# Performance work log

Measured on AMD Instinct MI355X. Metric: run time of the kernel, lower is better.

The kernel has to match this reference:

```python
import jax, jax.numpy as jnp
from jax import lax
import numpy as np

B, T, D_IN, H, OUT = 64, 512, 512, 1024, 128


def setup_inputs() -> dict:
    key = jax.random.key(0)
    ks = jax.random.split(key, 12)
    s = 0.02
    return {
        "x": jax.random.normal(ks[0], (B, T, D_IN), dtype=jnp.float32),
        "W_ih0": jax.random.normal(ks[1], (H, D_IN), dtype=jnp.float32) * s,
        "W_hh0": jax.random.normal(ks[2], (H, H), dtype=jnp.float32) * s,
        "b_ih0": jax.random.normal(ks[3], (H,), dtype=jnp.float32) * s,
        "b_hh0": jax.random.normal(ks[4], (H,), dtype=jnp.float32) * s,
        "W_ih1": jax.random.normal(ks[5], (H, H), dtype=jnp.float32) * s,
        "W_hh1": jax.random.normal(ks[6], (H, H), dtype=jnp.float32) * s,
        "b_ih1": jax.random.normal(ks[7], (H,), dtype=jnp.float32) * s,
        "b_hh1": jax.random.normal(ks[8], (H,), dtype=jnp.float32) * s,
        "W_fc": jax.random.normal(ks[9], (OUT, H), dtype=jnp.float32) * s,
        "b_fc": jax.random.normal(ks[10], (OUT,), dtype=jnp.float32) * s,
    }


def _rnn_layer(seq, W_ih, W_hh, b_ih, b_hh):
    # seq: [B, T, D] -> outputs [B, T, H]; h_t = tanh(x_t W_ih^T + b_ih + h_{t-1} W_hh^T + b_hh)
    pre = jnp.einsum("btd,hd->bth", seq, W_ih) + b_ih + b_hh  # one big input GEMM
    h0 = jnp.zeros((seq.shape[0], W_hh.shape[0]), dtype=seq.dtype)

    def step(h, p_t):
        h_new = jnp.tanh(p_t + h @ W_hh.T)
        return h_new, h_new

    _, hs = lax.scan(step, h0, jnp.swapaxes(pre, 0, 1))  # [T, B, H]
    return jnp.swapaxes(hs, 0, 1)  # [B, T, H]


def reference(x, W_ih0, W_hh0, b_ih0, b_hh0, W_ih1, W_hh1, b_ih1, b_hh1, W_fc, b_fc):
    h1 = _rnn_layer(x, W_ih0, W_hh0, b_ih0, b_hh0)
    h2 = _rnn_layer(h1, W_ih1, W_hh1, b_ih1, b_hh1)
    last = h2[:, -1, :]  # [B, H]
    return last @ W_fc.T + b_fc  # [B, OUT]
```

## Files before the change

kernel.cpp:

```cpp
#include <hip/hip_runtime.h>
#include <stdint.h>
#include <stddef.h>

#define Bn   64
#define Tn   512
#define DINn 512
#define Hn   1024
#define OUTn 128

typedef __attribute__((ext_vector_type(4))) float f32x4;
typedef __attribute__((ext_vector_type(8))) short short8;
typedef __attribute__((ext_vector_type(4))) unsigned int u32x4;

__device__ __forceinline__ unsigned short f2bf(float f){
  unsigned int x = __builtin_bit_cast(unsigned int, f);
  x += 0x7fffu + ((x >> 16) & 1u);
  return (unsigned short)(x >> 16);
}
__device__ __forceinline__ float bf2f(unsigned short u){
  return __builtin_bit_cast(float, (unsigned int)u << 16);
}
__device__ __forceinline__ float tanh_fast(float v){
  float e = __expf(2.0f * v);
  return 1.0f - 2.0f / (e + 1.0f);
}

template<bool FAST>
__device__ __forceinline__ void st16(unsigned short* p, u32x4 v){
  if constexpr (FAST)
    asm volatile("global_store_dwordx4 %0, %1, off sc0" :: "v"(p), "v"(v) : "memory");
  else
    asm volatile("global_store_dwordx4 %0, %1, off sc0 sc1" :: "v"(p), "v"(v) : "memory");
}
__device__ __forceinline__ unsigned atom_poll(unsigned int* p){
  unsigned old, zero = 0;
  asm volatile("global_atomic_add %0, %1, %2, off sc0\n\t"
               "s_waitcnt vmcnt(0)"
               : "=&v"(old) : "v"(p), "v"(zero) : "memory");
  return old;
}
__device__ __forceinline__ void atom_poll2(unsigned int* p1, unsigned int* p2,
                                           unsigned &v1, unsigned &v2){
  unsigned zero = 0;
  asm volatile("global_atomic_add %0, %2, %4, off sc0\n\t"
               "global_atomic_add %1, %3, %4, off sc0\n\t"
               "s_waitcnt vmcnt(0)"
               : "=&v"(v1), "=&v"(v2)
               : "v"(p1), "v"(p2), "v"(zero) : "memory");
}
__device__ __forceinline__ void atom_inc(unsigned int* p){
  unsigned one = 1;
  asm volatile("global_atomic_add %0, %1, off" :: "v"(p), "v"(one) : "memory");
}
__device__ __forceinline__ unsigned ld1_sc0(const unsigned int* p){
  unsigned v;
  asm volatile("global_load_dword %0, %1, off sc0\n\t"
               "s_waitcnt vmcnt(0)" : "=&v"(v) : "v"(p) : "memory");
  return v;
}
__device__ __forceinline__ unsigned ld1_nt(const unsigned int* p){
  unsigned v;
  asm volatile("global_load_dword %0, %1, off nt\n\t"
               "s_waitcnt vmcnt(0)" : "=&v"(v) : "v"(p) : "memory");
  return v;
}
__device__ __forceinline__ unsigned umin4(u32x4 a){
  unsigned m0 = a[0] < a[1] ? a[0] : a[1];
  unsigned m1 = a[2] < a[3] ? a[2] : a[3];
  return m0 < m1 ? m0 : m1;
}
__device__ __forceinline__ unsigned ld_line8_slow(const unsigned int* p){
  u32x4 a, b;
  asm volatile("global_load_dwordx4 %0, %2, off sc0 sc1\n\t"
               "global_load_dwordx4 %1, %3, off sc0 sc1\n\t"
               "s_waitcnt vmcnt(0)"
               : "=&v"(a), "=&v"(b) : "v"(p), "v"(p + 4) : "memory");
  unsigned ma = umin4(a), mb = umin4(b);
  return ma < mb ? ma : mb;
}
__device__ __forceinline__ unsigned ld_line8_nt(const unsigned int* p){
  u32x4 a, b;
  asm volatile("global_load_dwordx4 %0, %2, off nt\n\t"
               "global_load_dwordx4 %1, %3, off nt\n\t"
               "s_waitcnt vmcnt(0)"
               : "=&v"(a), "=&v"(b) : "v"(p), "v"(p + 4) : "memory");
  unsigned ma = umin4(a), mb = umin4(b);
  return ma < mb ? ma : mb;
}
__device__ __forceinline__ void wait8_nt(const unsigned int* p, unsigned want){
  if (!want) return;
  for (int i = 0; i < (1 << 16); ++i){
    if (ld_line8_nt(p) >= want) return;
    if (i > 8) __builtin_amdgcn_s_sleep(1);
  }
}
__device__ __forceinline__ void wait8_nt2(const unsigned int* p1, unsigned w1,
                                          const unsigned int* p2, unsigned w2){
  if (!w2){ wait8_nt(p1, w1); return; }
  for (int i = 0; i < (1 << 16); ++i){
    u32x4 a, b, c, d;
    asm volatile("global_load_dwordx4 %0, %4, off nt\n\t"
                 "global_load_dwordx4 %1, %5, off nt\n\t"
                 "global_load_dwordx4 %2, %6, off nt\n\t"
                 "global_load_dwordx4 %3, %7, off nt\n\t"
                 "s_waitcnt vmcnt(0)"
                 : "=&v"(a), "=&v"(b), "=&v"(c), "=&v"(d)
                 : "v"(p1), "v"(p1 + 4), "v"(p2), "v"(p2 + 4) : "memory");
    unsigned m1 = umin4(a) < umin4(b) ? umin4(a) : umin4(b);
    unsigned m2 = umin4(c) < umin4(d) ? umin4(c) : umin4(d);
    if (m1 >= w1 && m2 >= w2) return;
    if (i > 8) __builtin_amdgcn_s_sleep(1);
  }
}
template<bool FAST>
__device__ __forceinline__ void wait_one(unsigned int* fc, unsigned int* fl, unsigned wfast, unsigned wslow){
  if constexpr (FAST){
    if (!wfast) return;
    for (int i = 0; i < (1 << 16); ++i){
      if (atom_poll(fc) >= wfast) return;
      if (i > 8) __builtin_amdgcn_s_sleep(1);
    }
  } else {
    if (!wslow) return;
    for (int i = 0; i < (1 << 16); ++i){
      if (ld_line8_slow(fl) >= wslow) return;
      if (i > 16) __builtin_amdgcn_s_sleep(1);
    }
  }
}
template<bool FAST>
__device__ __forceinline__ void wait_dual(unsigned int* fc1, unsigned int* fl1, unsigned wf1, unsigned ws1,
                                          unsigned int* fc2, unsigned int* fl2, unsigned wf2, unsigned ws2){
  if constexpr (FAST){
    if (!wf2){ wait_one<true>(fc1, fl1, wf1, ws1); return; }
    for (int i = 0; i < (1 << 16); ++i){
      unsigned v1, v2;
      atom_poll2(fc1, fc2, v1, v2);
      if (v1 >= wf1 && v2 >= wf2) return;
      if (i > 8) __builtin_amdgcn_s_sleep(1);
    }
  } else {
    if (!ws2){ wait_one<false>(fc1, fl1, wf1, ws1); return; }
    for (int i = 0; i < (1 << 16); ++i){
      if (ld_line8_slow(fl1) >= ws1 && ld_line8_slow(fl2) >= ws2) return;
      if (i > 16) __builtin_amdgcn_s_sleep(1);
    }
  }
}

template<bool FAST>
__device__ __forceinline__ void stage_lin(const unsigned short* base, unsigned short* hl, int tid){
  const unsigned short* p0 = base + (size_t)tid * 8;
  const unsigned short* p1 = p0 + 4096;
  u32x4 v0, v1;
  if constexpr (FAST)
    asm volatile("global_load_dwordx4 %0, %2, off sc0\n\t"
                 "global_load_dwordx4 %1, %3, off sc0\n\t"
                 "s_waitcnt vmcnt(0)"
                 : "=&v"(v0), "=&v"(v1) : "v"(p0), "v"(p1) : "memory");
  else
    asm volatile("global_load_dwordx4 %0, %2, off sc0 sc1\n\t"
                 "global_load_dwordx4 %1, %3, off sc0 sc1\n\t"
                 "s_waitcnt vmcnt(0)"
                 : "=&v"(v0), "=&v"(v1) : "v"(p0), "v"(p1) : "memory");
  *(u32x4*)((char*)hl + tid * 16) = v0;
  *(u32x4*)((char*)hl + tid * 16 + 8192) = v1;
}
template<bool FAST>
__device__ __forceinline__ void ld4_chunk(const unsigned short* p, float* pv){
  unsigned u0,u1,u2,u3;
  if constexpr (FAST)
    asm volatile("global_load_ushort %0, %4, off sc0\n\t"
                 "global_load_ushort %1, %5, off sc0\n\t"
                 "global_load_ushort %2, %6, off sc0\n\t"
                 "global_load_ushort %3, %7, off sc0\n\t"
                 "s_waitcnt vmcnt(0)"
                 : "=&v"(u0), "=&v"(u1), "=&v"(u2), "=&v"(u3)
                 : "v"(p), "v"(p + 8), "v"(p + 16), "v"(p + 24) : "memory");
  else
    asm volatile("global_load_ushort %0, %4, off sc0 sc1\n\t"
                 "global_load_ushort %1, %5, off sc0 sc1\n\t"
                 "global_load_ushort %2, %6, off sc0 sc1\n\t"
                 "global_load_ushort %3, %7, off sc0 sc1\n\t"
                 "s_waitcnt vmcnt(0)"
                 : "=&v"(u0), "=&v"(u1), "=&v"(u2), "=&v"(u3)
                 : "v"(p), "v"(p + 8), "v"(p + 16), "v"(p + 24) : "memory");
  pv[0] = bf2f((unsigned short)u0); pv[1] = bf2f((unsigned short)u1);
  pv[2] = bf2f((unsigned short)u2); pv[3] = bf2f((unsigned short)u3);
}

__device__ __forceinline__ f32x4 mfma_tile(const char* lbase, const short8* wf, int lrow, int kh){
  f32x4 a0 = {0.f,0.f,0.f,0.f}, a1 = a0, a2 = a0, a3 = a0;
  int rb = kh * 128 + lrow * 16;
#pragma unroll
  for (int kk = 0; kk < 8; ++kk)
    a0 = __builtin_amdgcn_mfma_f32_16x16x32_bf16(*(const short8*)(lbase + kk*512 + rb), wf[kk], a0, 0,0,0);
#pragma unroll
  for (int kk = 8; kk < 16; ++kk)
    a1 = __builtin_amdgcn_mfma_f32_16x16x32_bf16(*(const short8*)(lbase + kk*512 + rb), wf[kk], a1, 0,0,0);
#pragma unroll
  for (int kk = 16; kk < 24; ++kk)
    a2 = __builtin_amdgcn_mfma_f32_16x16x32_bf16(*(const short8*)(lbase + kk*512 + rb), wf[kk], a2, 0,0,0);
#pragma unroll
  for (int kk = 24; kk < 32; ++kk)
    a3 = __builtin_amdgcn_mfma_f32_16x16x32_bf16(*(const short8*)(lbase + kk*512 + rb), wf[kk], a3, 0,0,0);
  return (a0 + a1) + (a2 + a3);
}

__global__ void cvt_bf16x8(const float* __restrict__ in, unsigned short* __restrict__ out,
                           long long n8){
  long long i = (long long)blockIdx.x * blockDim.x + threadIdx.x;
  long long stride = (long long)gridDim.x * blockDim.x;
  for (; i < n8; i += stride){
    const float* p = in + i*8;
    float4 a = *(const float4*)p;
    float4 b = *(const float4*)(p+4);
    short8 v;
    v[0]=(short)f2bf(a.x); v[1]=(short)f2bf(a.y); v[2]=(short)f2bf(a.z); v[3]=(short)f2bf(a.w);
    v[4]=(short)f2bf(b.x); v[5]=(short)f2bf(b.y); v[6]=(short)f2bf(b.z); v[7]=(short)f2bf(b.w);
    *(short8*)(out + i*8) = v;
  }
}

__global__ void bias_combine(const float* __restrict__ a, const float* __restrict__ b, float* __restrict__ o,
                             const float* __restrict__ c, const float* __restrict__ d, float* __restrict__ p){
  int i = blockIdx.x * blockDim.x + threadIdx.x;
  if (i < Hn){ o[i] = a[i] + b[i]; p[i] = c[i] + d[i]; }
}

__launch_bounds__(256, 2)
__global__ void gemm_pre0(const float* __restrict__ Av, const unsigned short* __restrict__ Bm,
                          const float* __restrict__ bias, unsigned short* __restrict__ C,
                          int N, int K)
{
  __shared__ unsigned short lA[128*64];
  __shared__ unsigned short lB[128*64];
  int bn = blockIdx.x, bm = blockIdx.y;
  int m0 = bm*128, n0 = bn*128;
  int tid = threadIdx.x, lane = tid & 63, w = tid >> 6;
  int wm = (w >> 1)*64, wn = (w & 1)*64;
  int cl = lane & 15, kh = lane >> 4;

  f32x4 acc[4][4];
  f32x4 z = {0.f,0.f,0.f,0.f};
#pragma unroll
  for (int i=0;i<4;i++)
#pragma unroll
    for (int j=0;j<4;j++) acc[i][j]=z;

  for (int k0 = 0; k0 < K; k0 += 64){
    __syncthreads();
#pragma unroll
    for (int r = 0; r < 4; ++r){
      int c = r*256 + tid;
      int row = c >> 3, cof = (c & 7)*8;
      const float* ap = Av + (size_t)(m0+row)*K + k0 + cof;
      float4 a = *(const float4*)ap;
      float4 b = *(const float4*)(ap+4);
      short8 v;
      v[0]=(short)f2bf(a.x); v[1]=(short)f2bf(a.y); v[2]=(short)f2bf(a.z); v[3]=(short)f2bf(a.w);
      v[4]=(short)f2bf(b.x); v[5]=(short)f2bf(b.y); v[6]=(short)f2bf(b.z); v[7]=(short)f2bf(b.w);
      *(short8*)&lA[row*64 + cof] = v;
      const unsigned short* bp = Bm + (size_t)(n0+row)*K + k0 + cof;
      *(short8*)&lB[row*64 + cof] = *(const short8*)bp;
    }
    __syncthreads();
#pragma unroll
    for (int kk = 0; kk < 2; ++kk){
      int kb = kk*32 + kh*8;
      short8 af[4], bfr[4];
#pragma unroll
      for (int i=0;i<4;i++) af[i]  = *(const short8*)&lA[(wm + i*16 + cl)*64 + kb];
#pragma unroll
      for (int j=0;j<4;j++) bfr[j] = *(const short8*)&lB[(wn + j*16 + cl)*64 + kb];
#pragma unroll
      for (int i=0;i<4;i++)
#pragma unroll
        for (int j=0;j<4;j++)
          acc[i][j] = __builtin_amdgcn_mfma_f32_16x16x32_bf16(af[i], bfr[j], acc[i][j], 0,0,0);
    }
  }
#pragma unroll
  for (int j=0;j<4;j++){
    int n = n0 + wn + j*16 + cl;
    float bs = bias[n];
#pragma unroll
    for (int i=0;i<4;i++){
      int mr = m0 + wm + i*16 + kh*4;
#pragma unroll
      for (int e=0;e<4;e++){
        int m = mr + e;
        int b = m >> 9, t = m & (Tn-1);
        C[((size_t)t*Bn + b)*N + n] = f2bf(acc[i][j][e] + bs);
      }
    }
  }
}

template<int MODE>
__device__ __forceinline__ void rnn_body(
    int role, int g, int slot, int tid, int w, int lane, int cl, int kh, int lrow,
    const unsigned short* pre0, unsigned short* bufP, unsigned short* h1buf,
    const float* bias1,
    unsigned int* FCA0, unsigned int* FCA1, unsigned int* FCB, unsigned int* FCC,
    unsigned int* FLA, unsigned int* FLB, unsigned int* FLC,
    unsigned int* FNA, unsigned int* FNB, unsigned int* FNC,
    const short8* wf, unsigned short* hl, unsigned short* outl)
{
  constexpr bool FAST = (MODE < 2);
  const char* lbase = (const char*)hl;
  int n0 = slot*128 + w*16;
  int olocal = w*128 + ((cl>>3)*8 + kh*4)*8 + (cl&7);
  unsigned int* myFL = ((role == 0) ? FLA : (role == 1) ? FLB : FLC) + slot;
  unsigned int* myFN = ((role == 0) ? FNA : (role == 1) ? FNB : FNC) + slot;

  for (int t = 0; t < Tn; ++t){
    float pv[4] = {0.f,0.f,0.f,0.f};
    if (role == 0 && kh < 2){
      const unsigned short* pp = pre0 + ((size_t)t*Bn + g*8 + kh*4)*Hn + n0 + cl;
#pragma unroll
      for (int j=0;j<4;j++) pv[j] = bf2f(pp[(size_t)j*Hn]);
    }
    if (tid == 0){
      if constexpr (MODE == 0){
        if (role == 0)      wait8_nt(FNA, (unsigned)t);
        else if (role == 1) wait8_nt(FNA, (unsigned)(t+1));
        else                wait8_nt2(FNB, (unsigned)(t+1), FNC, (unsigned)t);
      } else {
        if (role == 0)      wait_one <FAST>(FCA0, FLA, 8u*(unsigned)t, (unsigned)t);
        else if (role == 1) wait_one <FAST>(FCA1, FLA, 8u*(unsigned)(t+1), (unsigned)(t+1));
        else                wait_dual<FAST>(FCB, FLB, 8u*(unsigned)(t+1), (unsigned)(t+1),
                                            FCC, FLC, 8u*(unsigned)t, (unsigned)t);
      }
    }
    __syncthreads();
    bool staged = true;
    if (role == 0){
      if (t > 0) stage_lin<FAST>(h1buf + ((size_t)(t+1)*8 + g)*8192, hl, tid);
      else staged = false;
    } else if (role == 1){
      stage_lin<FAST>(h1buf + ((size_t)(t+2)*8 + g)*8192, hl, tid);
    } else {
      if (kh < 2)
        ld4_chunk<FAST>(h1buf + ((size_t)t*8 + g)*8192 + slot*1024 + ((w*16+cl)>>3)*64 + kh*32 + (cl&7), pv);
      if (t > 0) stage_lin<FAST>(bufP + ((size_t)(t-1)*Bn + g*8)*Hn, hl, tid);
      else staged = false;
    }
    __syncthreads();
    f32x4 acc = {0.f,0.f,0.f,0.f};
    if (staged) acc = mfma_tile(lbase, wf, lrow, kh);
    if (kh < 2){
      float bs = (role == 1) ? bias1[n0 + cl] : 0.f;
#pragma unroll
      for (int j=0;j<4;j++){
        float v = acc[j] + pv[j] + bs;
        if (role != 1) v = tanh_fast(v);
        outl[olocal + j*8] = f2bf(v);
      }
    }
    unsigned short* tile;
    if (role == 0)      tile = h1buf + ((size_t)(t+2)*8 + g)*8192;
    else if (role == 1) tile = h1buf + ((size_t)t*8 + g)*8192;
    else                tile = bufP + ((size_t)t*Bn + g*8)*Hn;
    if (lane < 16){
      u32x4 v = *(const u32x4*)(outl + w*128 + lane*8);
      st16<FAST>(tile + slot*1024 + (w*16 + lane)*8, v);
    }
    asm volatile("s_waitcnt vmcnt(0)" ::: "memory");
    __syncthreads();
    if (tid == 0){
      if constexpr (MODE == 0){
        asm volatile("global_store_dword %0, %1, off sc0" :: "v"(myFN), "v"((unsigned)(t+1)) : "memory");
      } else if constexpr (MODE == 1){
        if (role == 0){ atom_inc(FCA0); atom_inc(FCA1); }
        else if (role == 1) atom_inc(FCB);
        else atom_inc(FCC);
      } else {
        asm volatile("global_store_dword %0, %1, off sc0 sc1" :: "v"(myFL), "v"((unsigned)(t+1)) : "memory");
      }
    }
  }
}

__launch_bounds__(512, 2)
__global__ void rnn_fused(const unsigned short* __restrict__ pre0_ro,
                          unsigned short* __restrict__ bufP,
                          unsigned short* __restrict__ h1buf,
                          const float* __restrict__ Whh0,
                          const float* __restrict__ Wih1,
                          const float* __restrict__ Whh1,
                          const float* __restrict__ bias1,
                          unsigned int* ctrs)
{
  __shared__ __align__(16) unsigned short hl[8192];
  __shared__ __align__(16) unsigned short outl[1024];
  __shared__ int s_mode;
  int bx = blockIdx.x;
  int g = bx & 7;
  int sub = bx >> 3;
  int role = sub >> 3, slot = sub & 7;
  int tid = threadIdx.x, lane = tid & 63, w = tid >> 6;
  int n0 = slot*128 + w*16;
  int cl = lane & 15, kh = lane >> 4, lrow = cl & 7;
  unsigned int* FLA = ctrs + (0*8 + g)*32;
  unsigned int* FLB = ctrs + (1*8 + g)*32;
  unsigned int* FLC = ctrs + (2*8 + g)*32;
  unsigned int* arrive1 = ctrs + 768;
  unsigned int* badAT   = ctrs + 772;
  unsigned int* arrive2 = ctrs + 776;
  unsigned int* badNT   = ctrs + 780;
  unsigned int* arrive3 = ctrs + 784;
  unsigned int* FCA0 = ctrs + 1536 + (0*8 + g)*32;
  unsigned int* FCB  = ctrs + 1536 + (1*8 + g)*32;
  unsigned int* FCC  = ctrs + 1536 + (2*8 + g)*32;
  unsigned int* FCA1 = ctrs + 1536 + (3*8 + g)*32;
  unsigned int* FNA = ctrs + 2560 + (0*8 + g)*32;
  unsigned int* FNB = ctrs + 2560 + (1*8 + g)*32;
  unsigned int* FNC = ctrs + 2560 + (2*8 + g)*32;

  if (tid == 0){
    int xcc;
    asm volatile("s_getreg_b32 %0, hwreg(HW_REG_XCC_ID)" : "=s"(xcc));
    unsigned int* atw = ctrs + 1024 + g*32;  unsigned int* atarmed = atw + 16;
    unsigned int* ntw = ctrs + 3328 + g*32;  unsigned int* ntarmed = ntw + 16;
    if (xcc != g){
      __hip_atomic_fetch_or(badNT, 1u, __ATOMIC_RELAXED, __HIP_MEMORY_SCOPE_AGENT);
      __hip_atomic_fetch_or(badAT, 1u, __ATOMIC_RELAXED, __HIP_MEMORY_SCOPE_AGENT);
    }
    unsigned pr = ld1_nt(ntw) + ld1_nt(ntarmed);
    asm volatile("" :: "v"(pr));
    __hip_atomic_fetch_add(arrive1, 1u, __ATOMIC_ACQ_REL, __HIP_MEMORY_SCOPE_AGENT);
    int t1 = 0;
    for (int i = 0; i < (1 << 20); ++i){
      if (__hip_atomic_load(arrive1, __ATOMIC_ACQUIRE, __HIP_MEMORY_SCOPE_AGENT) >= 192u){ t1 = 1; break; }
      __builtin_amdgcn_s_sleep(2);
    }
    if (!t1){
      __hip_atomic_fetch_or(badNT, 1u, __ATOMIC_RELAXED, __HIP_MEMORY_SCOPE_AGENT);
      __hip_atomic_fetch_or(badAT, 1u, __ATOMIC_RELAXED, __HIP_MEMORY_SCOPE_AGENT);
    }
    unsigned magicN = 0xBEEF0000u | (unsigned)g;
    if (sub == 0){
      asm volatile("global_store_dword %0, %1, off sc0\n\t"
                   "s_waitcnt vmcnt(0)\n\t"
                   "global_store_dword %2, %3, off sc0"
                   :: "v"(ntw), "v"(magicN), "v"(ntarmed), "v"(1u) : "memory");
    }
    int okN = 0;
    for (int i = 0; i < (1 << 14); ++i){
      if (ld1_nt(ntarmed) == 1u){ okN = (ld1_nt(ntw) == magicN); break; }
      if (i > 8) __builtin_amdgcn_s_sleep(1);
    }
    if (!okN) __hip_atomic_fetch_or(badNT, 1u, __ATOMIC_RELAXED, __HIP_MEMORY_SCOPE_AGENT);
    __hip_atomic_fetch_add(arrive2, 1u, __ATOMIC_ACQ_REL, __HIP_MEMORY_SCOPE_AGENT);
    int t2 = 0;
    for (int i = 0; i < (1 << 20); ++i){
      if (__hip_atomic_load(arrive2, __ATOMIC_ACQUIRE, __HIP_MEMORY_SCOPE_AGENT) >= 192u){ t2 = 1; break; }
      __builtin_amdgcn_s_sleep(2);
    }
    if (!t2){
      __hip_atomic_fetch_or(badNT, 1u, __ATOMIC_RELAXED, __HIP_MEMORY_SCOPE_AGENT);
      __hip_atomic_fetch_or(badAT, 1u, __ATOMIC_RELAXED, __HIP_MEMORY_SCOPE_AGENT);
    }
    unsigned magicA = 0xCAFE0000u | (unsigned)g;
    if (sub == 0){
      asm volatile("global_store_dword %0, %1, off sc0\n\t"
                   "s_waitcnt vmcnt(0)" :: "v"(atw), "v"(magicA) : "memory");
      atom_inc(atarmed);
    }
    int okA = 0;
    for (int i = 0; i < (1 << 15); ++i){
      if (atom_poll(atarmed) >= 1u){ okA = (ld1_sc0(atw) == magicA); break; }
      if (i > 16) __builtin_amdgcn_s_sleep(1);
    }
    if (!okA) __hip_atomic_fetch_or(badAT, 1u, __ATOMIC_RELAXED, __HIP_MEMORY_SCOPE_AGENT);
    __hip_atomic_fetch_add(arrive3, 1u, __ATOMIC_ACQ_REL, __HIP_MEMORY_SCOPE_AGENT);
    int t3 = 0;
    for (int i = 0; i < (1 << 20); ++i){
      if (__hip_atomic_load(arrive3, __ATOMIC_ACQUIRE, __HIP_MEMORY_SCOPE_AGENT) >= 192u){ t3 = 1; break; }
      __builtin_amdgcn_s_sleep(2);
    }
    unsigned bN = __hip_atomic_load(badNT, __ATOMIC_ACQUIRE, __HIP_MEMORY_SCOPE_AGENT);
    unsigned bA = __hip_atomic_load(badAT, __ATOMIC_ACQUIRE, __HIP_MEMORY_SCOPE_AGENT);
    s_mode = (!t3) ? 2 : (bN == 0u ? 0 : (bA == 0u ? 1 : 2));
  }
  __syncthreads();
  const int mode = s_mode;

  const float* Wmat = (role == 0) ? Whh0 : (role == 1) ? Wih1 : Whh1;
  short8 wf[32];
  {
    const float* wr = Wmat + (size_t)(n0 + cl)*Hn + kh*8;
#pragma unroll
    for (int kk = 0; kk < 32; ++kk){
      float4 a = *(const float4*)(wr + kk*32);
      float4 b = *(const float4*)(wr + kk*32 + 4);
      short8 v;
      v[0]=(short)f2bf(a.x); v[1]=(short)f2bf(a.y); v[2]=(short)f2bf(a.z); v[3]=(short)f2bf(a.w);
      v[4]=(short)f2bf(b.x); v[5]=(short)f2bf(b.y); v[6]=(short)f2bf(b.z); v[7]=(short)f2bf(b.w);
      wf[kk] = v;
    }
  }

  if (mode == 0)
    rnn_body<0>(role, g, slot, tid, w, lane, cl, kh, lrow, pre0_ro, bufP, h1buf,
                bias1, FCA0, FCA1, FCB, FCC, FLA, FLB, FLC, FNA, FNB, FNC, wf, hl, outl);
  else if (mode == 1)
    rnn_body<1>(role, g, slot, tid, w, lane, cl, kh, lrow, pre0_ro, bufP, h1buf,
                bias1, FCA0, FCA1, FCB, FCC, FLA, FLB, FLC, FNA, FNB, FNC, wf, hl, outl);
  else
    rnn_body<2>(role, g, slot, tid, w, lane, cl, kh, lrow, pre0_ro, bufP, h1buf,
                bias1, FCA0, FCA1, FCB, FCC, FLA, FLB, FLC, FNA, FNB, FNC, wf, hl, outl);
}

__global__ void fc_k(const unsigned short* __restrict__ bufP,
                     const float* __restrict__ Wfc, const float* __restrict__ bfc,
                     float* __restrict__ out)
{
  int gw = (blockIdx.x * blockDim.x + threadIdx.x) >> 6;
  int lane = threadIdx.x & 63;
  int b = gw >> 7, o = gw & 127;
  const unsigned short* tile = bufP + ((size_t)(Tn-1)*Bn + (b & ~7))*Hn;
  int r = b & 7;
  const float* wr = Wfc + (size_t)o*Hn;
  float s = 0.f;
  for (int k = lane; k < Hn; k += 64)
    s += bf2f(tile[((k>>3)*8 + r)*8 + (k&7)]) * wr[k];
#pragma unroll
  for (int off = 32; off > 0; off >>= 1) s += __shfl_down(s, off, 64);
  if (lane == 0) out[b*OUTn + o] = s + bfc[o];
}

extern "C" void kernel_launch(void* const* d_in, const int* in_sizes, int n_in,
                              void* d_out, int out_size, void* d_ws, size_t ws_size,
                              hipStream_t stream)
{
  const float* x    = (const float*)d_in[0];
  const float* Wih0 = (const float*)d_in[1];
  const float* Whh0 = (const float*)d_in[2];
  const float* bih0 = (const float*)d_in[3];
  const float* bhh0 = (const float*)d_in[4];
  const float* Wih1 = (const float*)d_in[5];
  const float* Whh1 = (const float*)d_in[6];
  const float* bih1 = (const float*)d_in[7];
  const float* bhh1 = (const float*)d_in[8];
  const float* Wfc  = (const float*)d_in[9];
  const float* bfc  = (const float*)d_in[10];
  float* out = (float*)d_out;

  unsigned short* bufP  = (unsigned short*)d_ws;
  unsigned short* h1buf = bufP  + (size_t)Bn*Tn*Hn;
  unsigned short* wih0b = h1buf + (size_t)(Tn+2)*8*8192;
  float* bias0 = (float*)(wih0b + (size_t)Hn*DINn);
  float* bias1 = bias0 + Hn;
  unsigned int* ctrs = (unsigned int*)(bias1 + Hn);

  hipMemsetAsync(ctrs, 0, 4096*sizeof(unsigned int), stream);

  cvt_bf16x8<<<256, 256, 0, stream>>>(Wih0, wih0b, (long long)Hn*DINn/8);
  bias_combine<<<4, 256, 0, stream>>>(bih0, bhh0, bias0, bih1, bhh1, bias1);

  dim3 g1(Hn/128, (Bn*Tn)/128);
  gemm_pre0<<<g1, 256, 0, stream>>>(x, wih0b, bias0, bufP, Hn, DINn);

  rnn_fused<<<192, 512, 0, stream>>>(bufP, bufP, h1buf, Whh0, Wih1, Whh1, bias1, ctrs);

  fc_k<<<2048, 256, 0, stream>>>(bufP, Wfc, bfc, out);
}
```

Baseline: 1.199 ms.

## Split K across warp halves with two column tiles per warp and LDS reduction

Each warp now computes two 16-column output tiles over half of the K dimension, reusing every LDS A-fragment for two MFMAs instead of one. Partial sums from the upper four warps go through a new LDS reduction buffer, adding an extra barrier per timestep. The per-step h1 gather loads for role 2 are merged into the same inline-asm batch as the tile staging loads, so one wait covers both. The aim is to halve LDS fragment reads and shorten each timestep's critical path. The cost is an additional __syncthreads and some extra register pressure.

```diff
diff --git a/kernel.cpp b/kernel.cpp
--- a/kernel.cpp
+++ b/kernel.cpp
@@ -165,6 +165,52 @@
                  : "=&v"(v0), "=&v"(v1) : "v"(p0), "v"(p1) : "memory");
   *(u32x4*)((char*)hl + tid * 16) = v0;
   *(u32x4*)((char*)hl + tid * 16 + 8192) = v1;
+}
+template<bool FAST>
+__device__ __forceinline__ void stage_ld8(const unsigned short* base, unsigned short* hl, int tid,
+                                          const unsigned short* pA, const unsigned short* pB,
+                                          float* pvA, float* pvB){
+  const unsigned short* p0 = base + (size_t)tid * 8;
+  const unsigned short* p1 = p0 + 4096;
+  u32x4 v0, v1; unsigned a0,a1,a2,a3,b0,b1,b2,b3;
+  if constexpr (FAST)
+    asm volatile(
+      "global_load_dwordx4 %0, %10, off sc0\n\t"
+      "global_load_dwordx4 %1, %11, off sc0\n\t"
+      "global_load_ushort %2, %12, off sc0\n\t"
+      "global_load_ushort %3, %13, off sc0\n\t"
+      "global_load_ushort %4, %14, off sc0\n\t"
+      "global_load_ushort %5, %15, off sc0\n\t"
+      "global_load_ushort %6, %16, off sc0\n\t"
+      "global_load_ushort %7, %17, off sc0\n\t"
+      "global_load_ushort %8, %18, off sc0\n\t"
+      "global_load_ushort %9, %19, off sc0\n\t"
+      "s_waitcnt vmcnt(0)"
+      : "=&v"(v0),"=&v"(v1),"=&v"(a0),"=&v"(a1),"=&v"(a2),"=&v"(a3),"=&v"(b0),"=&v"(b1),"=&v"(b2),"=&v"(b3)
+      : "v"(p0),"v"(p1),"v"(pA),"v"(pA+8),"v"(pA+16),"v"(pA+24),"v"(pB),"v"(pB+8),"v"(pB+16),"v"(pB+24)
+      : "memory");
+  else
+    asm volatile(
+      "global_load_dwordx4 %0, %10, off sc0 sc1\n\t"
+      "global_load_dwordx4 %1, %11, off sc0 sc1\n\t"
+      "global_load_ushort %2, %12, off sc0 sc1\n\t"
+      "global_load_ushort %3, %13, off sc0 sc1\n\t"
+      "global_load_ushort %4, %14, off sc0 sc1\n\t"
+      "global_load_ushort %5, %15, off sc0 sc1\n\t"
+      "global_load_ushort %6, %16, off sc0 sc1\n\t"
+      "global_load_ushort %7, %17, off sc0 sc1\n\t"
+      "global_load_ushort %8, %18, off sc0 sc1\n\t"
+      "global_load_ushort %9, %19, off sc0 sc1\n\t"
+      "s_waitcnt vmcnt(0)"
+      : "=&v"(v0),"=&v"(v1),"=&v"(a0),"=&v"(a1),"=&v"(a2),"=&v"(a3),"=&v"(b0),"=&v"(b1),"=&v"(b2),"=&v"(b3)
+      : "v"(p0),"v"(p1),"v"(pA),"v"(pA+8),"v"(pA+16),"v"(pA+24),"v"(pB),"v"(pB+8),"v"(pB+16),"v"(pB+24)
+      : "memory");
+  *(u32x4*)((char*)hl + tid * 16) = v0;
+  *(u32x4*)((char*)hl + tid * 16 + 8192) = v1;
+  pvA[0]=bf2f((unsigned short)a0); pvA[1]=bf2f((unsigned short)a1);
+  pvA[2]=bf2f((unsigned short)a2); pvA[3]=bf2f((unsigned short)a3);
+  pvB[0]=bf2f((unsigned short)b0); pvB[1]=bf2f((unsigned short)b1);
+  pvB[2]=bf2f((unsigned short)b2); pvB[3]=bf2f((unsigned short)b3);
 }
 template<bool FAST>
 __device__ __forceinline__ void ld4_chunk(const unsigned short* p, float* pv){
@@ -189,24 +235,6 @@
   pv[2] = bf2f((unsigned short)u2); pv[3] = bf2f((unsigned short)u3);
 }
 
-__device__ __forceinline__ f32x4 mfma_tile(const char* lbase, const short8* wf, int lrow, int kh){
-  f32x4 a0 = {0.f,0.f,0.f,0.f}, a1 = a0, a2 = a0, a3 = a0;
-  int rb = kh * 128 + lrow * 16;
-#pragma unroll
-  for (int kk = 0; kk < 8; ++kk)
-    a0 = __builtin_amdgcn_mfma_f32_16x16x32_bf16(*(const short8*)(lbase + kk*512 + rb), wf[kk], a0, 0,0,0);
-#pragma unroll
-  for (int kk = 8; kk < 16; ++kk)
-    a1 = __builtin_amdgcn_mfma_f32_16x16x32_bf16(*(const short8*)(lbase + kk*512 + rb), wf[kk], a1, 0,0,0);
-#pragma unroll
-  for (int kk = 16; kk < 24; ++kk)
-    a2 = __builtin_amdgcn_mfma_f32_16x16x32_bf16(*(const short8*)(lbase + kk*512 + rb), wf[kk], a2, 0,0,0);
-#pragma unroll
-  for (int kk = 24; kk < 32; ++kk)
-    a3 = __builtin_amdgcn_mfma_f32_16x16x32_bf16(*(const short8*)(lbase + kk*512 + rb), wf[kk], a3, 0,0,0);
-  return (a0 + a1) + (a2 + a3);
-}
-
 __global__ void cvt_bf16x8(const float* __restrict__ in, unsigned short* __restrict__ out,
                            long long n8){
   long long i = (long long)blockIdx.x * blockDim.x + threadIdx.x;
@@ -305,21 +333,29 @@
     unsigned int* FCA0, unsigned int* FCA1, unsigned int* FCB, unsigned int* FCC,
     unsigned int* FLA, unsigned int* FLB, unsigned int* FLC,
     unsigned int* FNA, unsigned int* FNB, unsigned int* FNC,
-    const short8* wf, unsigned short* hl, unsigned short* outl)
+    const short8* wfA, const short8* wfB, unsigned short* hl, unsigned short* outl,
+    f32x4* red)
 {
   constexpr bool FAST = (MODE < 2);
   const char* lbase = (const char*)hl;
-  int n0 = slot*128 + w*16;
-  int olocal = w*128 + ((cl>>3)*8 + kh*4)*8 + (cl&7);
+  int t0 = 2*(w & 3);
+  int kb = (w >> 2) * 16;
+  int khc = kh & 1;
+  int oA = t0*128 + ((cl>>3)*8 + kh*4)*8 + (cl&7);
   unsigned int* myFL = ((role == 0) ? FLA : (role == 1) ? FLB : FLC) + slot;
   unsigned int* myFN = ((role == 0) ? FNA : (role == 1) ? FNB : FNC) + slot;
+  float bsA = 0.f, bsB = 0.f;
+  if (role == 1 && w < 4){
+    bsA = bias1[slot*128 + t0*16 + cl];
+    bsB = bias1[slot*128 + (t0+1)*16 + cl];
+  }
 
   for (int t = 0; t < Tn; ++t){
-    float pv[4] = {0.f,0.f,0.f,0.f};
-    if (role == 0 && kh < 2){
-      const unsigned short* pp = pre0 + ((size_t)t*Bn + g*8 + kh*4)*Hn + n0 + cl;
-#pragma unroll
-      for (int j=0;j<4;j++) pv[j] = bf2f(pp[(size_t)j*Hn]);
+    float pvA[4] = {0.f,0.f,0.f,0.f}, pvB[4] = {0.f,0.f,0.f,0.f};
+    if (role == 0 && w < 4 && kh < 2){
+      const unsigned short* pp = pre0 + ((size_t)t*Bn + g*8 + kh*4)*Hn + slot*128 + t0*16 + cl;
+#pragma unroll
+      for (int j=0;j<4;j++){ pvA[j] = bf2f(pp[(size_t)j*Hn]); pvB[j] = bf2f(pp[(size_t)j*Hn + 16]); }
     }
     if (tid == 0){
       if constexpr (MODE == 0){
@@ -341,30 +377,58 @@
     } else if (role == 1){
       stage_lin<FAST>(h1buf + ((size_t)(t+2)*8 + g)*8192, hl, tid);
     } else {
-      if (kh < 2)
-        ld4_chunk<FAST>(h1buf + ((size_t)t*8 + g)*8192 + slot*1024 + ((w*16+cl)>>3)*64 + kh*32 + (cl&7), pv);
-      if (t > 0) stage_lin<FAST>(bufP + ((size_t)(t-1)*Bn + g*8)*Hn, hl, tid);
-      else staged = false;
+      const unsigned short* pb = h1buf + ((size_t)t*8 + g)*8192 + slot*1024;
+      const unsigned short* pA = pb + (t0*2 + (cl>>3))*64 + khc*32 + (cl&7);
+      const unsigned short* pB = pb + ((t0+1)*2 + (cl>>3))*64 + khc*32 + (cl&7);
+      if (t > 0){
+        if (w < 4) stage_ld8<FAST>(bufP + ((size_t)(t-1)*Bn + g*8)*Hn, hl, tid, pA, pB, pvA, pvB);
+        else       stage_lin<FAST>(bufP + ((size_t)(t-1)*Bn + g*8)*Hn, hl, tid);
+      } else {
+        staged = false;
+        if (w < 4){ ld4_chunk<FAST>(pA, pvA); ld4_chunk<FAST>(pB, pvB); }
+      }
     }
     __syncthreads();
-    f32x4 acc = {0.f,0.f,0.f,0.f};
-    if (staged) acc = mfma_tile(lbase, wf, lrow, kh);
-    if (kh < 2){
-      float bs = (role == 1) ? bias1[n0 + cl] : 0.f;
-#pragma unroll
-      for (int j=0;j<4;j++){
-        float v = acc[j] + pv[j] + bs;
-        if (role != 1) v = tanh_fast(v);
-        outl[olocal + j*8] = f2bf(v);
-      }
-    }
-    unsigned short* tile;
-    if (role == 0)      tile = h1buf + ((size_t)(t+2)*8 + g)*8192;
-    else if (role == 1) tile = h1buf + ((size_t)t*8 + g)*8192;
-    else                tile = bufP + ((size_t)t*Bn + g*8)*Hn;
-    if (lane < 16){
-      u32x4 v = *(const u32x4*)(outl + w*128 + lane*8);
-      st16<FAST>(tile + slot*1024 + (w*16 + lane)*8, v);
+    f32x4 zz = {0.f,0.f,0.f,0.f};
+    f32x4 accA = zz, accB = zz;
+    if (staged){
+      const char* fp = lbase + kb*512 + kh*128 + lrow*16;
+#pragma unroll
+      for (int q = 0; q < 16; ++q){
+        short8 a = *(const short8*)(fp + q*512);
+        accA = __builtin_amdgcn_mfma_f32_16x16x32_bf16(a, wfA[q], accA, 0,0,0);
+        accB = __builtin_amdgcn_mfma_f32_16x16x32_bf16(a, wfB[q], accB, 0,0,0);
+      }
+    }
+    if (w >= 4 && kh < 2){
+      red[t0*32 + kh*16 + cl]       = accA;
+      red[(t0+1)*32 + kh*16 + cl]   = accB;
+    }
+    __syncthreads();
+    if (w < 4){
+      if (kh < 2){
+        accA += red[t0*32 + kh*16 + cl];
+        accB += red[(t0+1)*32 + kh*16 + cl];
+        float bs0 = (role == 1) ? bsA : 0.f;
+        float bs1 = (role == 1) ? bsB : 0.f;
+#pragma unroll
+        for (int j=0;j<4;j++){
+          float vA = accA[j] + pvA[j] + bs0;
+          float vB = accB[j] + pvB[j] + bs1;
+          if (role != 1){ vA = tanh_fast(vA); vB = tanh_fast(vB); }
+          outl[oA + j*8]       = f2bf(vA);
+          outl[oA + 128 + j*8] = f2bf(vB);
+        }
+      }
+      unsigned short* tile;
+      if (role == 0)      tile = h1buf + ((size_t)(t+2)*8 + g)*8192;
+      else if (role == 1) tile = h1buf + ((size_t)t*8 + g)*8192;
+      else                tile = bufP + ((size_t)t*Bn + g*8)*Hn;
+      tile += slot*1024;
+      if (lane < 16){
+        st16<FAST>(tile + (t0*16 + lane)*8,     *(const u32x4*)(outl + t0*128 + lane*8));
+        st16<FAST>(tile + ((t0+1)*16 + lane)*8, *(const u32x4*)(outl + (t0+1)*128 + lane*8));
+      }
     }
     asm volatile("s_waitcnt vmcnt(0)" ::: "memory");
     __syncthreads();
@@ -394,13 +458,13 @@
 {
   __shared__ __align__(16) unsigned short hl[8192];
   __shared__ __align__(16) unsigned short outl[1024];
+  __shared__ __align__(16) f32x4 red[256];
   __shared__ int s_mode;
   int bx = blockIdx.x;
   int g = bx & 7;
   int sub = bx >> 3;
   int role = sub >> 3, slot = sub & 7;
   int tid = threadIdx.x, lane = tid & 63, w = tid >> 6;
-  int n0 = slot*128 + w*16;
   int cl = lane & 15, kh = lane >> 4, lrow = cl & 7;
   unsigned int* FLA = ctrs + (0*8 + g)*32;
   unsigned int* FLB = ctrs + (1*8 + g)*32;
@@ -488,29 +552,42 @@
   const int mode = s_mode;
 
   const float* Wmat = (role == 0) ? Whh0 : (role == 1) ? Wih1 : Whh1;
-  short8 wf[32];
+  int t0 = 2*(w & 3);
+  int kb = (w >> 2) * 16;
+  short8 wfA[16], wfB[16];
   {
-    const float* wr = Wmat + (size_t)(n0 + cl)*Hn + kh*8;
-#pragma unroll
-    for (int kk = 0; kk < 32; ++kk){
-      float4 a = *(const float4*)(wr + kk*32);
-      float4 b = *(const float4*)(wr + kk*32 + 4);
-      short8 v;
-      v[0]=(short)f2bf(a.x); v[1]=(short)f2bf(a.y); v[2]=(short)f2bf(a.z); v[3]=(short)f2bf(a.w);
-      v[4]=(short)f2bf(b.x); v[5]=(short)f2bf(b.y); v[6]=(short)f2bf(b.z); v[7]=(short)f2bf(b.w);
-      wf[kk] = v;
+    const float* wrA = Wmat + (size_t)(slot*128 + t0*16 + cl)*Hn + kb*32 + kh*8;
+    const float* wrB = wrA + (size_t)16*Hn;
+#pragma unroll
+    for (int q = 0; q < 16; ++q){
+      {
+        float4 a = *(const float4*)(wrA + q*32);
+        float4 b = *(const float4*)(wrA + q*32 + 4);
+        short8 v;
+        v[0]=(short)f2bf(a.x); v[1]=(short)f2bf(a.y); v[2]=(short)f2bf(a.z); v[3]=(short)f2bf(a.w);
+        v[4]=(short)f2bf(b.x); v[5]=(short)f2bf(b.y); v[6]=(short)f2bf(b.z); v[7]=(short)f2bf(b.w);
+        wfA[q] = v;
+      }
+      {
+        float4 a = *(const float4*)(wrB + q*32);
+        float4 b = *(const float4*)(wrB + q*32 + 4);
+        short8 v;
+        v[0]=(short)f2bf(a.x); v[1]=(short)f2bf(a.y); v[2]=(short)f2bf(a.z); v[3]=(short)f2bf(a.w);
+        v[4]=(short)f2bf(b.x); v[5]=(short)f2bf(b.y); v[6]=(short)f2bf(b.z); v[7]=(short)f2bf(b.w);
+        wfB[q] = v;
+      }
     }
   }
 
   if (mode == 0)
     rnn_body<0>(role, g, slot, tid, w, lane, cl, kh, lrow, pre0_ro, bufP, h1buf,
-                bias1, FCA0, FCA1, FCB, FCC, FLA, FLB, FLC, FNA, FNB, FNC, wf, hl, outl);
+                bias1, FCA0, FCA1, FCB, FCC, FLA, FLB, FLC, FNA, FNB, FNC, wfA, wfB, hl, outl, red);
   else if (mode == 1)
     rnn_body<1>(role, g, slot, tid, w, lane, cl, kh, lrow, pre0_ro, bufP, h1buf,
-                bias1, FCA0, FCA1, FCB, FCC, FLA, FLB, FLC, FNA, FNB, FNC, wf, hl, outl);
+                bias1, FCA0, FCA1, FCB, FCC, FLA, FLB, FLC, FNA, FNB, FNC, wfA, wfB, hl, outl, red);
   else
     rnn_body<2>(role, g, slot, tid, w, lane, cl, kh, lrow, pre0_ro, bufP, h1buf,
-                bias1, FCA0, FCA1, FCB, FCC, FLA, FLB, FLC, FNA, FNB, FNC, wf, hl, outl);
+                bias1, FCA0, FCA1, FCB, FCC, FLA, FLB, FLC, FNA, FNB, FNC, wfA, wfB, hl, outl, red);
 }
 
 __global__ void fc_k(const unsigned short* __restrict__ bufP,
```

Measured after the change: 1.313 ms. 1.1x slower.

## Use per-wave flag waits and per-wave staging in MODE 0 recurrence

Applied to the files above, without the earlier changes.

In MODE 0, each wave now polls only the single flag word for the slice it needs and stages its own 1024-element chunk of the hidden state into LDS. This replaces the tid-0 wait over a full 8-word flag line followed by a block-wide barrier and cooperative staging. The aim is to remove one __syncthreads per timestep and let each wave start as soon as its own producer is done. The role-2 path also fuses the pre-activation loads into the staging load. In exchange every wave now spins on global memory, and correctness relies on the finer-grained producer/consumer flag mapping being right.

```diff
diff --git a/kernel.cpp b/kernel.cpp
--- a/kernel.cpp
+++ b/kernel.cpp
@@ -64,6 +64,13 @@
                "s_waitcnt vmcnt(0)" : "=&v"(v) : "v"(p) : "memory");
   return v;
 }
+__device__ __forceinline__ void ld2_nt(const unsigned int* p1, const unsigned int* p2,
+                                       unsigned &v1, unsigned &v2){
+  asm volatile("global_load_dword %0, %2, off nt\n\t"
+               "global_load_dword %1, %3, off nt\n\t"
+               "s_waitcnt vmcnt(0)"
+               : "=&v"(v1), "=&v"(v2) : "v"(p1), "v"(p2) : "memory");
+}
 __device__ __forceinline__ unsigned umin4(u32x4 a){
   unsigned m0 = a[0] < a[1] ? a[0] : a[1];
   unsigned m1 = a[2] < a[3] ? a[2] : a[3];
@@ -78,38 +85,21 @@
   unsigned ma = umin4(a), mb = umin4(b);
   return ma < mb ? ma : mb;
 }
-__device__ __forceinline__ unsigned ld_line8_nt(const unsigned int* p){
-  u32x4 a, b;
-  asm volatile("global_load_dwordx4 %0, %2, off nt\n\t"
-               "global_load_dwordx4 %1, %3, off nt\n\t"
-               "s_waitcnt vmcnt(0)"
-               : "=&v"(a), "=&v"(b) : "v"(p), "v"(p + 4) : "memory");
-  unsigned ma = umin4(a), mb = umin4(b);
-  return ma < mb ? ma : mb;
-}
-__device__ __forceinline__ void wait8_nt(const unsigned int* p, unsigned want){
+__device__ __forceinline__ void waitw_nt(const unsigned int* p, unsigned want){
   if (!want) return;
   for (int i = 0; i < (1 << 16); ++i){
-    if (ld_line8_nt(p) >= want) return;
-    if (i > 8) __builtin_amdgcn_s_sleep(1);
-  }
-}
-__device__ __forceinline__ void wait8_nt2(const unsigned int* p1, unsigned w1,
+    if (ld1_nt(p) >= want) return;
+    if (i > 16) __builtin_amdgcn_s_sleep(1);
+  }
+}
+__device__ __forceinline__ void waitw_nt2(const unsigned int* p1, unsigned w1,
                                           const unsigned int* p2, unsigned w2){
-  if (!w2){ wait8_nt(p1, w1); return; }
+  if (!w1){ waitw_nt(p2, w2); return; }
   for (int i = 0; i < (1 << 16); ++i){
-    u32x4 a, b, c, d;
-    asm volatile("global_load_dwordx4 %0, %4, off nt\n\t"
-                 "global_load_dwordx4 %1, %5, off nt\n\t"
-                 "global_load_dwordx4 %2, %6, off nt\n\t"
-                 "global_load_dwordx4 %3, %7, off nt\n\t"
-                 "s_waitcnt vmcnt(0)"
-                 : "=&v"(a), "=&v"(b), "=&v"(c), "=&v"(d)
-                 : "v"(p1), "v"(p1 + 4), "v"(p2), "v"(p2 + 4) : "memory");
-    unsigned m1 = umin4(a) < umin4(b) ? umin4(a) : umin4(b);
-    unsigned m2 = umin4(c) < umin4(d) ? umin4(c) : umin4(d);
-    if (m1 >= w1 && m2 >= w2) return;
-    if (i > 8) __builtin_amdgcn_s_sleep(1);
+    unsigned v1, v2;
+    ld2_nt(p1, p2, v1, v2);
+    if (v1 >= w1 && v2 >= w2) return;
+    if (i > 16) __builtin_amdgcn_s_sleep(1);
   }
 }
 template<bool FAST>
@@ -146,6 +136,38 @@
       if (i > 16) __builtin_amdgcn_s_sleep(1);
     }
   }
+}
+
+__device__ __forceinline__ void stage_pw(const unsigned short* src, unsigned short* dst, int lane){
+  const unsigned short* p0 = src + lane*8;
+  const unsigned short* p1 = p0 + 512;
+  u32x4 v0, v1;
+  asm volatile("global_load_dwordx4 %0, %2, off sc0\n\t"
+               "global_load_dwordx4 %1, %3, off sc0\n\t"
+               "s_waitcnt vmcnt(0)"
+               : "=&v"(v0), "=&v"(v1) : "v"(p0), "v"(p1) : "memory");
+  *(u32x4*)(dst + lane*8) = v0;
+  *(u32x4*)(dst + lane*8 + 512) = v1;
+}
+__device__ __forceinline__ void stage_pw_pv(const unsigned short* src, unsigned short* dst, int lane,
+                                            const unsigned short* p4, float* pv){
+  const unsigned short* p0 = src + lane*8;
+  const unsigned short* p1 = p0 + 512;
+  u32x4 v0, v1; unsigned u0,u1,u2,u3;
+  asm volatile(
+    "global_load_dwordx4 %0, %6, off sc0\n\t"
+    "global_load_dwordx4 %1, %7, off sc0\n\t"
+    "global_load_ushort %2, %8, off sc0\n\t"
+    "global_load_ushort %3, %9, off sc0\n\t"
+    "global_load_ushort %4, %10, off sc0\n\t"
+    "global_load_ushort %5, %11, off sc0\n\t"
+    "s_waitcnt vmcnt(0)"
+    : "=&v"(v0),"=&v"(v1),"=&v"(u0),"=&v"(u1),"=&v"(u2),"=&v"(u3)
+    : "v"(p0),"v"(p1),"v"(p4),"v"(p4+8),"v"(p4+16),"v"(p4+24) : "memory");
+  *(u32x4*)(dst + lane*8) = v0;
+  *(u32x4*)(dst + lane*8 + 512) = v1;
+  pv[0]=bf2f((unsigned short)u0); pv[1]=bf2f((unsigned short)u1);
+  pv[2]=bf2f((unsigned short)u2); pv[3]=bf2f((unsigned short)u3);
 }
 
 template<bool FAST>
@@ -311,6 +333,7 @@
   const char* lbase = (const char*)hl;
   int n0 = slot*128 + w*16;
   int olocal = w*128 + ((cl>>3)*8 + kh*4)*8 + (cl&7);
+  int khc = kh & 1;
   unsigned int* myFL = ((role == 0) ? FLA : (role == 1) ? FLB : FLC) + slot;
   unsigned int* myFN = ((role == 0) ? FNA : (role == 1) ? FNB : FNC) + slot;
 
@@ -321,30 +344,47 @@
 #pragma unroll
       for (int j=0;j<4;j++) pv[j] = bf2f(pp[(size_t)j*Hn]);
     }
-    if (tid == 0){
-      if constexpr (MODE == 0){
-        if (role == 0)      wait8_nt(FNA, (unsigned)t);
-        else if (role == 1) wait8_nt(FNA, (unsigned)(t+1));
-        else                wait8_nt2(FNB, (unsigned)(t+1), FNC, (unsigned)t);
+    bool staged = true;
+    if constexpr (MODE == 0){
+      if (role == 0){
+        if (t > 0){
+          waitw_nt(FNA + w, (unsigned)t);
+          stage_pw(h1buf + ((size_t)(t+1)*8 + g)*8192 + w*1024, hl + w*1024, lane);
+        } else staged = false;
+      } else if (role == 1){
+        waitw_nt(FNA + w, (unsigned)(t+1));
+        stage_pw(h1buf + ((size_t)(t+2)*8 + g)*8192 + w*1024, hl + w*1024, lane);
       } else {
+        const unsigned short* pA = h1buf + ((size_t)t*8 + g)*8192 + slot*1024
+                                   + ((w*16+cl)>>3)*64 + khc*32 + (cl&7);
+        if (t > 0){
+          waitw_nt2(FNC + w, (unsigned)t, FNB + slot, (unsigned)(t+1));
+          stage_pw_pv(bufP + ((size_t)(t-1)*Bn + g*8)*Hn + w*1024, hl + w*1024, lane, pA, pv);
+        } else {
+          staged = false;
+          waitw_nt(FNB + slot, 1u);
+          ld4_chunk<true>(pA, pv);
+        }
+      }
+    } else {
+      if (tid == 0){
         if (role == 0)      wait_one <FAST>(FCA0, FLA, 8u*(unsigned)t, (unsigned)t);
         else if (role == 1) wait_one <FAST>(FCA1, FLA, 8u*(unsigned)(t+1), (unsigned)(t+1));
         else                wait_dual<FAST>(FCB, FLB, 8u*(unsigned)(t+1), (unsigned)(t+1),
                                             FCC, FLC, 8u*(unsigned)t, (unsigned)t);
       }
-    }
-    __syncthreads();
-    bool staged = true;
-    if (role == 0){
-      if (t > 0) stage_lin<FAST>(h1buf + ((size_t)(t+1)*8 + g)*8192, hl, tid);
-      else staged = false;
-    } else if (role == 1){
-      stage_lin<FAST>(h1buf + ((size_t)(t+2)*8 + g)*8192, hl, tid);
-    } else {
-      if (kh < 2)
-        ld4_chunk<FAST>(h1buf + ((size_t)t*8 + g)*8192 + slot*1024 + ((w*16+cl)>>3)*64 + kh*32 + (cl&7), pv);
-      if (t > 0) stage_lin<FAST>(bufP + ((size_t)(t-1)*Bn + g*8)*Hn, hl, tid);
-      else staged = false;
+      __syncthreads();
+      if (role == 0){
+        if (t > 0) stage_lin<FAST>(h1buf + ((size_t)(t+1)*8 + g)*8192, hl, tid);
+        else staged = false;
+      } else if (role == 1){
+        stage_lin<FAST>(h1buf + ((size_t)(t+2)*8 + g)*8192, hl, tid);
+      } else {
+        if (kh < 2)
+          ld4_chunk<FAST>(h1buf + ((size_t)t*8 + g)*8192 + slot*1024 + ((w*16+cl)>>3)*64 + kh*32 + (cl&7), pv);
+        if (t > 0) stage_lin<FAST>(bufP + ((size_t)(t-1)*Bn + g*8)*Hn, hl, tid);
+        else staged = false;
+      }
     }
     __syncthreads();
     f32x4 acc = {0.f,0.f,0.f,0.f};
```

After: 1.148 ms, median of 2. 4.2% less time.
